# Performance work log

Hardware: AMD Instinct MI355X
Metric: run time of the kernel (lower is better)

Reference implementation:

```python
import jax, jax.numpy as jnp
import numpy as np

DEC = 1024
MEM = 1024


def setup_inputs() -> dict:
    key = jax.random.key(0)
    k1, k2, k3, k4, k5 = jax.random.split(key, 5)
    decoder_state = jax.random.normal(k1, (64, DEC), dtype=jnp.float32)
    memory_bank = jax.random.normal(k2, (64, 2048, MEM), dtype=jnp.float32)
    src_mask = jnp.ones((64, 2048), dtype=jnp.int32)
    # learned params (torch Linear: y = x @ W.T); store as (in, out) for einsum
    s = 1.0 / np.sqrt(DEC)
    W_v = jax.random.uniform(k3, (DEC,), jnp.float32, -s, s)            # v: decoder_size -> 1
    W_dec = jax.random.uniform(k4, (DEC, DEC), jnp.float32, -s, s)       # decode_project
    sm = 1.0 / np.sqrt(MEM)
    W_mem = jax.random.uniform(k5, (MEM, DEC), jnp.float32, -sm, sm)     # memory_project
    return {"decoder_state": decoder_state, "memory_bank": memory_bank,
            "src_mask": src_mask, "W_v": W_v, "W_dec": W_dec, "W_mem": W_mem}


def reference(decoder_state, memory_bank, src_mask, W_v, W_dec, W_mem):
    # encoder_feature: [B,S,D]; dec_feature: [B,D]
    enc_feat = jnp.einsum('bsm,md->bsd', memory_bank, W_mem)
    dec_feat = jnp.einsum('bm,md->bd', decoder_state, W_dec)
    e = jnp.tanh(enc_feat + dec_feat[:, None, :])      # [B,S,D]
    scores = jnp.einsum('bsd,d->bs', e, W_v)           # [B,S]
    scores = jnp.where(src_mask == 0, -jnp.inf, scores)
    attn_dist = jax.nn.softmax(scores, axis=-1)        # [B,S]
    context = jnp.einsum('bs,bsm->bm', attn_dist, memory_bank)  # [B,M]
    return (context, attn_dist)
```

## Files before the change

kernel.cpp:

```cpp
#include <hip/hip_runtime.h>

typedef __bf16 bf16;
typedef __bf16 bf16x8 __attribute__((ext_vector_type(8)));
typedef float f32x4 __attribute__((ext_vector_type(4)));

constexpr int kB = 64;
constexpr int kS = 2048;
constexpr int kD = 1024;
constexpr int kM = 1024;
constexpr int kRows = kB * kS;

__device__ __forceinline__ void async_copy16(const void* gsrc, void* ldst) {
    __builtin_amdgcn_global_load_lds(
        (const __attribute__((address_space(1))) void*)gsrc,
        (__attribute__((address_space(3))) void*)ldst, 16, 0, 0);
}

__device__ __forceinline__ float fast_tanh(float x) {
    float e = __expf(2.0f * x);
    return 1.0f - 2.0f * __builtin_amdgcn_rcpf(e + 1.0f);
}

__global__ __launch_bounds__(256) void wmem_transpose_kernel(
    const float* __restrict__ Wm, bf16* __restrict__ WT) {
    int idx = blockIdx.x * 256 + threadIdx.x;
    int d = idx >> 10, m = idx & 1023;
    WT[idx] = (bf16)Wm[m * 1024 + d];
}

__global__ __launch_bounds__(256) void dec_project_kernel(
    const float* __restrict__ dec, const float* __restrict__ Wd,
    float* __restrict__ decf) {
    const int b = blockIdx.x;
    const int d = blockIdx.y * 256 + threadIdx.x;
    const float* drow = dec + b * kD;
    float acc = 0.f;
    #pragma unroll 8
    for (int m = 0; m < kM; ++m)
        acc += drow[m] * Wd[(size_t)m * kD + d];
    decf[b * kD + d] = acc;
}

constexpr int BM = 128, BN = 256, BK = 32, APAD = 40;
constexpr int NCOL = kD / BN;

__global__ __launch_bounds__(512, 4) void attn_scores_kernel(
    const float* __restrict__ MBank,
    const bf16*  __restrict__ WT,
    const float* __restrict__ decf,
    const float* __restrict__ Wv,
    float* __restrict__ spart)
{
    __shared__ bf16 Atile[BM * APAD];
    __shared__ bf16 Btile[BN * BK];
    __shared__ float sred[BM * 4];

    const int tid  = threadIdx.x;
    const int wave = tid >> 6;
    const int lane = tid & 63;
    const int ln   = lane & 15;
    const int quad = lane >> 4;

    const int L = blockIdx.y * NCOL + blockIdx.x;
    const int jw = L >> 3;
    const int rowTile = ((L & 7) << 7) + (jw >> 2);
    const int colTile = jw & 3;
    const int R0 = rowTile * BM;
    const int C0 = colTile * BN;
    const int batch = rowTile >> 4;

    const int wr = (wave >> 2) * 64;
    const int wc = (wave & 3) * 64;

    const int arow  = tid >> 2;
    const int akseg = (tid & 3) * 8;
    const float* aptr = MBank + (size_t)(R0 + arow) * kM + akseg;

    f32x4 acc[4][4];
    const f32x4 zero = {0.f, 0.f, 0.f, 0.f};
    #pragma unroll
    for (int i = 0; i < 4; ++i)
        #pragma unroll
        for (int j = 0; j < 4; ++j)
            acc[i][j] = zero;

    for (int k0 = 0; k0 < kM; k0 += BK) {
        __syncthreads();
        #pragma unroll
        for (int jj = 0; jj < 2; ++jj) {
            const int chunk = wave * 2 + jj;
            const int n = chunk * 16 + (lane >> 2);
            async_copy16(WT + (size_t)(C0 + n) * kM + k0 + (lane & 3) * 8,
                         Btile + chunk * 512);
        }
        {
            const float* ap = aptr + k0;
            f32x4 v0 = *(const f32x4*)(ap + 0);
            f32x4 v1 = *(const f32x4*)(ap + 4);
            bf16x8 w0;
            w0[0]=(bf16)v0[0]; w0[1]=(bf16)v0[1]; w0[2]=(bf16)v0[2]; w0[3]=(bf16)v0[3];
            w0[4]=(bf16)v1[0]; w0[5]=(bf16)v1[1]; w0[6]=(bf16)v1[2]; w0[7]=(bf16)v1[3];
            *(bf16x8*)(Atile + arow * APAD + akseg) = w0;
        }
        __syncthreads();

        bf16x8 af[4], bfr[4];
        #pragma unroll
        for (int i = 0; i < 4; ++i)
            af[i] = *(const bf16x8*)(Atile + (wr + i * 16 + ln) * APAD + quad * 8);
        #pragma unroll
        for (int j = 0; j < 4; ++j)
            bfr[j] = *(const bf16x8*)(Btile + (wc + j * 16 + ln) * BK + quad * 8);
        #pragma unroll
        for (int i = 0; i < 4; ++i)
            #pragma unroll
            for (int j = 0; j < 4; ++j)
                acc[i][j] = __builtin_amdgcn_mfma_f32_16x16x32_bf16(
                    af[i], bfr[j], acc[i][j], 0, 0, 0);
    }

    float wv[4], df[4];
    #pragma unroll
    for (int j = 0; j < 4; ++j) {
        const int d = C0 + wc + j * 16 + ln;
        wv[j] = Wv[d];
        df[j] = decf[batch * kD + d];
    }
    float rp[4][4];
    #pragma unroll
    for (int i = 0; i < 4; ++i) {
        #pragma unroll
        for (int r = 0; r < 4; ++r) {
            float p = 0.f;
            #pragma unroll
            for (int j = 0; j < 4; ++j) {
                float x = acc[i][j][r] + df[j];
                p += fast_tanh(x) * wv[j];
            }
            #pragma unroll
            for (int off = 1; off < 16; off <<= 1)
                p += __shfl_xor(p, off, 64);
            rp[i][r] = p;
        }
    }
    if (ln == 0) {
        #pragma unroll
        for (int i = 0; i < 4; ++i)
            #pragma unroll
            for (int r = 0; r < 4; ++r)
                sred[(wr + i * 16 + quad * 4 + r) * 4 + (wave & 3)] = rp[i][r];
    }
    __syncthreads();
    if (tid < BM)
        spart[(size_t)colTile * kRows + R0 + tid] =
            (sred[tid * 4 + 0] + sred[tid * 4 + 1]) +
            (sred[tid * 4 + 2] + sred[tid * 4 + 3]);
}

__global__ __launch_bounds__(256) void softmax_kernel(
    const float* __restrict__ spart, const int* __restrict__ mask,
    float* __restrict__ attn) {
    const int b = blockIdx.x;
    const int tid = threadIdx.x;
    __shared__ float sc[kS];
    __shared__ float redm[4], reds[4];

    float lmax = -INFINITY;
    for (int s = tid; s < kS; s += 256) {
        float v = 0.f;
        #pragma unroll
        for (int t = 0; t < NCOL; ++t) v += spart[(size_t)t * kRows + b * kS + s];
        if (mask[b * kS + s] == 0) v = -INFINITY;
        sc[s] = v;
        lmax = fmaxf(lmax, v);
    }
    #pragma unroll
    for (int off = 32; off; off >>= 1) lmax = fmaxf(lmax, __shfl_xor(lmax, off, 64));
    if ((tid & 63) == 0) redm[tid >> 6] = lmax;
    __syncthreads();
    const float bmax = fmaxf(fmaxf(redm[0], redm[1]), fmaxf(redm[2], redm[3]));

    float lsum = 0.f;
    for (int s = tid; s < kS; s += 256) {
        float e = __expf(sc[s] - bmax);
        sc[s] = e;
        lsum += e;
    }
    #pragma unroll
    for (int off = 32; off; off >>= 1) lsum += __shfl_xor(lsum, off, 64);
    if ((tid & 63) == 0) reds[tid >> 6] = lsum;
    __syncthreads();
    const float inv = 1.0f / (reds[0] + reds[1] + reds[2] + reds[3]);
    for (int s = tid; s < kS; s += 256) attn[b * kS + s] = sc[s] * inv;
}

__global__ __launch_bounds__(256) void ctx_partial_kernel(
    const float* __restrict__ MBank, const float* __restrict__ attn,
    float* __restrict__ cpart) {
    const int b  = blockIdx.x;
    const int sc = blockIdx.y;
    const int m4 = threadIdx.x * 4;
    const float* base = MBank + ((size_t)b * kS + sc * 128) * kM + m4;
    const float* ap = attn + b * kS + sc * 128;
    f32x4 acc = {0.f, 0.f, 0.f, 0.f};
    #pragma unroll 4
    for (int s = 0; s < 128; ++s) {
        const float a = ap[s];
        f32x4 v = *(const f32x4*)(base + (size_t)s * kM);
        acc[0] += a * v[0]; acc[1] += a * v[1];
        acc[2] += a * v[2]; acc[3] += a * v[3];
    }
    *(f32x4*)&cpart[((size_t)(b * 16 + sc)) * kM + m4] = acc;
}

__global__ __launch_bounds__(256) void ctx_reduce_kernel(
    const float* __restrict__ cpart, float* __restrict__ out) {
    const int idx = blockIdx.x * 256 + threadIdx.x;
    const int b = idx >> 10, m = idx & 1023;
    float v = 0.f;
    #pragma unroll
    for (int c = 0; c < 16; ++c) v += cpart[(size_t)((b * 16 + c) << 10) + m];
    out[idx] = v;
}

extern "C" void kernel_launch(void* const* d_in, const int* in_sizes, int n_in,
                              void* d_out, int out_size, void* d_ws, size_t ws_size,
                              hipStream_t stream) {
    const float* dec   = (const float*)d_in[0];
    const float* MBank = (const float*)d_in[1];
    const int*   mask  = (const int*)d_in[2];
    const float* Wv    = (const float*)d_in[3];
    const float* Wdec  = (const float*)d_in[4];
    const float* Wmem  = (const float*)d_in[5];

    float* out_ctx  = (float*)d_out;
    float* out_attn = (float*)d_out + kB * kD;

    char* ws = (char*)d_ws;
    bf16*  WT    = (bf16*)ws;
    float* decf  = (float*)(ws + (1 << 21));
    float* spart = (float*)(ws + (1 << 21) + (1 << 18));
    float* cpart = (float*)(ws + (1 << 21) + (1 << 18) + (1 << 21));

    wmem_transpose_kernel<<<4096, 256, 0, stream>>>(Wmem, WT);
    dec_project_kernel<<<dim3(64, 4), 256, 0, stream>>>(dec, Wdec, decf);
    attn_scores_kernel<<<dim3(NCOL, 1024), 512, 0, stream>>>(MBank, WT, decf, Wv, spart);
    softmax_kernel<<<64, 256, 0, stream>>>(spart, mask, out_attn);
    ctx_partial_kernel<<<dim3(64, 16), 256, 0, stream>>>(MBank, out_attn, cpart);
    ctx_reduce_kernel<<<256, 256, 0, stream>>>(cpart, out_ctx);
}
```

Measured before the change: 1.156 ms.

## Double-buffer GEMM tiles, tile the W_mem transpose, split context accumulators

The scores GEMM now double-buffers its A and B LDS tiles. The next k-step's global loads and async copies are issued before the current MFMAs run, which leaves one barrier per step and lets memory latency overlap with compute, and s_setprio is raised around the MFMA block. The W_mem transpose goes through a shared-memory tile so both reads and writes are coalesced. The context partial kernel uses two independent accumulators to expose more ILP. The cost is double the LDS footprint, which may reduce occupancy.

```diff
diff --git a/kernel.cpp b/kernel.cpp
--- a/kernel.cpp
+++ b/kernel.cpp
@@ -23,9 +23,22 @@
 
 __global__ __launch_bounds__(256) void wmem_transpose_kernel(
     const float* __restrict__ Wm, bf16* __restrict__ WT) {
-    int idx = blockIdx.x * 256 + threadIdx.x;
-    int d = idx >> 10, m = idx & 1023;
-    WT[idx] = (bf16)Wm[m * 1024 + d];
+    __shared__ bf16 tile[64][72];
+    const int d0 = (blockIdx.x & 15) * 64;
+    const int m0 = (blockIdx.x >> 4) * 64;
+    const int lane = threadIdx.x & 63;
+    const int grp  = threadIdx.x >> 6;
+    #pragma unroll
+    for (int r = 0; r < 16; ++r) {
+        const int m = m0 + grp * 16 + r;
+        tile[lane][grp * 16 + r] = (bf16)Wm[m * 1024 + d0 + lane];
+    }
+    __syncthreads();
+    #pragma unroll
+    for (int r = 0; r < 16; ++r) {
+        const int d = d0 + grp * 16 + r;
+        WT[d * 1024 + m0 + lane] = tile[grp * 16 + r][lane];
+    }
 }
 
 __global__ __launch_bounds__(256) void dec_project_kernel(
@@ -43,6 +56,7 @@
 
 constexpr int BM = 128, BN = 256, BK = 32, APAD = 40;
 constexpr int NCOL = kD / BN;
+constexpr int NSTEP = kM / BK;
 
 __global__ __launch_bounds__(512, 4) void attn_scores_kernel(
     const float* __restrict__ MBank,
@@ -51,8 +65,8 @@
     const float* __restrict__ Wv,
     float* __restrict__ spart)
 {
-    __shared__ bf16 Atile[BM * APAD];
-    __shared__ bf16 Btile[BN * BK];
+    __shared__ bf16 Abuf[2][BM * APAD];
+    __shared__ bf16 Bbuf[2][BN * BK];
     __shared__ float sred[BM * 4];
 
     const int tid  = threadIdx.x;
@@ -76,6 +90,27 @@
     const int akseg = (tid & 3) * 8;
     const float* aptr = MBank + (size_t)(R0 + arow) * kM + akseg;
 
+    const int bn0   = (lane >> 2);
+    const int bkoff = (lane & 3) * 8;
+
+    {
+        const float* ap = aptr;
+        f32x4 v0 = *(const f32x4*)(ap + 0);
+        f32x4 v1 = *(const f32x4*)(ap + 4);
+        #pragma unroll
+        for (int jj = 0; jj < 2; ++jj) {
+            const int chunk = wave * 2 + jj;
+            const int n = chunk * 16 + bn0;
+            async_copy16(WT + (size_t)(C0 + n) * kM + bkoff,
+                         Bbuf[0] + chunk * 512);
+        }
+        bf16x8 w0;
+        w0[0]=(bf16)v0[0]; w0[1]=(bf16)v0[1]; w0[2]=(bf16)v0[2]; w0[3]=(bf16)v0[3];
+        w0[4]=(bf16)v1[0]; w0[5]=(bf16)v1[1]; w0[6]=(bf16)v1[2]; w0[7]=(bf16)v1[3];
+        *(bf16x8*)(Abuf[0] + arow * APAD + akseg) = w0;
+    }
+    __syncthreads();
+
     f32x4 acc[4][4];
     const f32x4 zero = {0.f, 0.f, 0.f, 0.f};
     #pragma unroll
@@ -84,39 +119,51 @@
         for (int j = 0; j < 4; ++j)
             acc[i][j] = zero;
 
-    for (int k0 = 0; k0 < kM; k0 += BK) {
-        __syncthreads();
-        #pragma unroll
-        for (int jj = 0; jj < 2; ++jj) {
-            const int chunk = wave * 2 + jj;
-            const int n = chunk * 16 + (lane >> 2);
-            async_copy16(WT + (size_t)(C0 + n) * kM + k0 + (lane & 3) * 8,
-                         Btile + chunk * 512);
+    #pragma unroll 2
+    for (int t = 0; t < NSTEP; ++t) {
+        const int cur = t & 1, nxt = cur ^ 1;
+        const bool pf = (t + 1 < NSTEP);
+        const int k1 = (t + 1) * BK;
+
+        f32x4 v0, v1;
+        if (pf) {
+            const float* ap = aptr + k1;
+            v0 = *(const f32x4*)(ap + 0);
+            v1 = *(const f32x4*)(ap + 4);
+            #pragma unroll
+            for (int jj = 0; jj < 2; ++jj) {
+                const int chunk = wave * 2 + jj;
+                const int n = chunk * 16 + bn0;
+                async_copy16(WT + (size_t)(C0 + n) * kM + k1 + bkoff,
+                             Bbuf[nxt] + chunk * 512);
+            }
         }
-        {
-            const float* ap = aptr + k0;
-            f32x4 v0 = *(const f32x4*)(ap + 0);
-            f32x4 v1 = *(const f32x4*)(ap + 4);
+
+        const bf16* Ac = Abuf[cur];
+        const bf16* Bc = Bbuf[cur];
+        bf16x8 af[4], bfr[4];
+        #pragma unroll
+        for (int i = 0; i < 4; ++i)
+            af[i] = *(const bf16x8*)(Ac + (wr + i * 16 + ln) * APAD + quad * 8);
+        #pragma unroll
+        for (int j = 0; j < 4; ++j)
+            bfr[j] = *(const bf16x8*)(Bc + (wc + j * 16 + ln) * BK + quad * 8);
+        __builtin_amdgcn_s_setprio(1);
+        #pragma unroll
+        for (int i = 0; i < 4; ++i)
+            #pragma unroll
+            for (int j = 0; j < 4; ++j)
+                acc[i][j] = __builtin_amdgcn_mfma_f32_16x16x32_bf16(
+                    af[i], bfr[j], acc[i][j], 0, 0, 0);
+        __builtin_amdgcn_s_setprio(0);
+
+        if (pf) {
             bf16x8 w0;
             w0[0]=(bf16)v0[0]; w0[1]=(bf16)v0[1]; w0[2]=(bf16)v0[2]; w0[3]=(bf16)v0[3];
             w0[4]=(bf16)v1[0]; w0[5]=(bf16)v1[1]; w0[6]=(bf16)v1[2]; w0[7]=(bf16)v1[3];
-            *(bf16x8*)(Atile + arow * APAD + akseg) = w0;
+            *(bf16x8*)(Abuf[nxt] + arow * APAD + akseg) = w0;
         }
         __syncthreads();
-
-        bf16x8 af[4], bfr[4];
-        #pragma unroll
-        for (int i = 0; i < 4; ++i)
-            af[i] = *(const bf16x8*)(Atile + (wr + i * 16 + ln) * APAD + quad * 8);
-        #pragma unroll
-        for (int j = 0; j < 4; ++j)
-            bfr[j] = *(const bf16x8*)(Btile + (wc + j * 16 + ln) * BK + quad * 8);
-        #pragma unroll
-        for (int i = 0; i < 4; ++i)
-            #pragma unroll
-            for (int j = 0; j < 4; ++j)
-                acc[i][j] = __builtin_amdgcn_mfma_f32_16x16x32_bf16(
-                    af[i], bfr[j], acc[i][j], 0, 0, 0);
     }
 
     float wv[4], df[4];
@@ -202,15 +249,19 @@
     const int m4 = threadIdx.x * 4;
     const float* base = MBank + ((size_t)b * kS + sc * 128) * kM + m4;
     const float* ap = attn + b * kS + sc * 128;
-    f32x4 acc = {0.f, 0.f, 0.f, 0.f};
+    f32x4 acc0 = {0.f, 0.f, 0.f, 0.f};
+    f32x4 acc1 = {0.f, 0.f, 0.f, 0.f};
     #pragma unroll 4
-    for (int s = 0; s < 128; ++s) {
-        const float a = ap[s];
-        f32x4 v = *(const f32x4*)(base + (size_t)s * kM);
-        acc[0] += a * v[0]; acc[1] += a * v[1];
-        acc[2] += a * v[2]; acc[3] += a * v[3];
-    }
-    *(f32x4*)&cpart[((size_t)(b * 16 + sc)) * kM + m4] = acc;
+    for (int s = 0; s < 128; s += 2) {
+        const float a0 = ap[s];
+        const float a1 = ap[s + 1];
+        f32x4 u0 = *(const f32x4*)(base + (size_t)s * kM);
+        f32x4 u1 = *(const f32x4*)(base + (size_t)(s + 1) * kM);
+        acc0 += u0 * a0;
+        acc1 += u1 * a1;
+    }
+    f32x4 r = acc0 + acc1;
+    *(f32x4*)&cpart[((size_t)(b * 16 + sc)) * kM + m4] = r;
 }
 
 __global__ __launch_bounds__(256) void ctx_reduce_kernel(
@@ -242,7 +293,7 @@
     float* spart = (float*)(ws + (1 << 21) + (1 << 18));
     float* cpart = (float*)(ws + (1 << 21) + (1 << 18) + (1 << 21));
 
-    wmem_transpose_kernel<<<4096, 256, 0, stream>>>(Wmem, WT);
+    wmem_transpose_kernel<<<256, 256, 0, stream>>>(Wmem, WT);
     dec_project_kernel<<<dim3(64, 4), 256, 0, stream>>>(dec, Wdec, decf);
     attn_scores_kernel<<<dim3(NCOL, 1024), 512, 0, stream>>>(MBank, WT, decf, Wv, spart);
     softmax_kernel<<<64, 256, 0, stream>>>(spart, mask, out_attn);
```

Measured after the change: 1.135 ms. Within noise of the previous version (-1.8%).
